# Kernel tuning notes

Hardware: AMD Instinct MI355X
Metric: run time of the kernel (lower is better)

Reference implementation:

```python
import jax, jax.numpy as jnp
import numpy as np

BN_EPS = 1e-5


def setup_inputs() -> dict:
    key = jax.random.key(0)
    ks = jax.random.split(key, 11)
    C, P = 256, 128  # inplanes, planes = inplanes // 2
    B, H, W = 4, 64, 64
    s = 0.01  # conv weight init std in the original module
    return {
        "x": jax.random.normal(ks[0], (B, C, H, W), jnp.float32),
        "Wt": jax.random.normal(ks[1], (P, C), jnp.float32) * s,
        "bt": jnp.zeros((P,), jnp.float32),
        "Wp": jax.random.normal(ks[2], (P, C), jnp.float32) * s,
        "bp": jnp.zeros((P,), jnp.float32),
        "Wg": jax.random.normal(ks[3], (P, C), jnp.float32) * s,
        "bg": jnp.zeros((P,), jnp.float32),
        "Wz": jax.random.normal(ks[4], (C, P), jnp.float32) * s,
        "bz": jnp.zeros((C,), jnp.float32),
        "gamma": jax.random.uniform(ks[5], (C,), jnp.float32),
        "beta": jax.random.normal(ks[6], (C,), jnp.float32) * 0.01,
    }


def reference(x, Wt, bt, Wp, bp, Wg, bg, Wz, bz, gamma, beta):
    b, c, h, w = x.shape
    n = h * w
    xf = x.reshape(b, c, n)  # (b, c, n)
    # 1x1 conv projections == per-pixel matmuls
    t = jnp.einsum("pc,bcn->bnp", Wt, xf) + bt            # (b, n, p) queries
    p = jnp.einsum("pc,bcn->bpn", Wp, xf) + bp[:, None]   # (b, p, n) keys
    g = jnp.einsum("pc,bcn->bnp", Wg, xf) + bg            # (b, n, p) values
    planes = Wt.shape[0]
    scale = jnp.asarray(planes, x.dtype) ** 0.5
    att = jnp.einsum("bnp,bpm->bnm", t, p) / scale        # (b, n, n)
    att = jax.nn.softmax(att, axis=-1)                    # softmax over dim 2
    y = jnp.einsum("bnm,bmp->bnp", att, g)                # (b, n, p)
    z = jnp.einsum("cp,bnp->bcn", Wz, y) + bz[:, None]    # (b, c, n)
    z = z.reshape(b, c, h, w)
    # BatchNorm2d, training-mode batch statistics over (B, H, W)
    mean = z.mean(axis=(0, 2, 3))
    var = z.var(axis=(0, 2, 3))
    zn = (z - mean[:, None, None]) * jax.lax.rsqrt(var + BN_EPS)[:, None, None]
    out = zn * gamma[:, None, None] + beta[:, None, None] + x
    return out
```

## Files before the change

kernel.cpp:

```cpp
#include <hip/hip_runtime.h>


#define SCALE_ 0.08838834764831845f
#define SCALE2_ 0.12752740475999508f

typedef __bf16 bf16x8 __attribute__((ext_vector_type(8)));
typedef float f32x4 __attribute__((ext_vector_type(4)));
typedef unsigned short ushort8v __attribute__((ext_vector_type(8)));

__device__ inline unsigned short f2bf(float f) {
  unsigned int u = __float_as_uint(f);
  u += 0x7fffu + ((u >> 16) & 1u);
  return (unsigned short)(u >> 16);
}
__device__ inline float bflo(unsigned int u) { return __uint_as_float(u << 16); }
__device__ inline float bfhi(unsigned int u) { return __uint_as_float(u & 0xffff0000u); }

__device__ inline void gl16(const unsigned short* g, unsigned short* l) {
  __builtin_amdgcn_global_load_lds(
      (const __attribute__((address_space(1))) unsigned int*)(g),
      (__attribute__((address_space(3))) unsigned int*)(l), 16, 0, 0);
}

__global__ __launch_bounds__(256) void prep_kernel(
    const float* __restrict__ x,
    const float* __restrict__ Wt, const float* __restrict__ Wp, const float* __restrict__ Wg,
    unsigned short* __restrict__ xT, unsigned short* __restrict__ Wb) {
  const int tid = threadIdx.x;
  const int bx = blockIdx.x, b = blockIdx.y;
  if (bx >= 64) {
    if (b != 0) return;
#pragma unroll
    for (int it = 0; it < 3; ++it) {
      int k = (bx - 64) * 256 + tid + it * 4096;
      const float* src = (k < 4096 ? Wt : (k < 8192 ? Wp : Wg)) + (size_t)(k & 4095) * 8;
      float4 a = *(const float4*)src, c = *(const float4*)(src + 4);
      ushort8v us;
      us[0] = f2bf(a.x); us[1] = f2bf(a.y); us[2] = f2bf(a.z); us[3] = f2bf(a.w);
      us[4] = f2bf(c.x); us[5] = f2bf(c.y); us[6] = f2bf(c.z); us[7] = f2bf(c.w);
      *(ushort8v*)(Wb + (size_t)k * 8) = us;
    }
    return;
  }
  __shared__ float sT[128 * 68];
  const int w = tid >> 6, l = tid & 63;
  const int n0 = bx * 64;
  for (int half = 0; half < 2; ++half) {
    if (half) __syncthreads();
#pragma unroll
    for (int it = 0; it < 8; ++it) {
      int e = it * 256 + tid;
      int c = e >> 4, n4 = e & 15;
      float4 v = *(const float4*)(x + (size_t)(b * 256 + half * 128 + c) * 4096 + n0 + n4 * 4);
      *(float4*)(sT + c * 68 + n4 * 4) = v;
    }
    __syncthreads();
#pragma unroll
    for (int it = 0; it < 4; ++it) {
      int c8 = it * 4 + w;
      int n = l;
      ushort8v us;
#pragma unroll
      for (int j = 0; j < 8; ++j) us[j] = f2bf(sT[(c8 * 8 + j) * 68 + n]);
      *(ushort8v*)(xT + (size_t)b * 1048576 + (size_t)(n0 + n) * 256 + half * 128 + c8 * 8) = us;
    }
  }
}

__global__ __launch_bounds__(256, 3) void proj_kernel(
    const unsigned short* __restrict__ xT, const unsigned short* __restrict__ Wb,
    const float* __restrict__ bt, const float* __restrict__ bp, const float* __restrict__ bg,
    unsigned short* __restrict__ Qb, unsigned short* __restrict__ Kb,
    unsigned short* __restrict__ Vtb) {
  __shared__ unsigned short sX[64 * 256];
  __shared__ unsigned short sW[128 * 64];
  const int tid = threadIdx.x;
  const int w = tid >> 6, l = tid & 63;
  const int l15 = l & 15, lh = l >> 4;
  const int n0 = blockIdx.x * 64;
  const int b = blockIdx.y;
  const int sel = blockIdx.z;
  const unsigned short* xTb = xT + (size_t)b * 1048576;
  const unsigned short* Ws = Wb + (size_t)sel * 32768;
#pragma unroll
  for (int it = 0; it < 8; ++it) {
    int row = w * 16 + it * 2 + (l >> 5);
    int s = l & 31;
    int src = (s & 24) | ((s & 7) ^ (row & 7));
    gl16(xTb + (size_t)(n0 + row) * 256 + src * 8, sX + (w * 16 + it * 2) * 256);
  }
  f32x4 acc[2][4];
#pragma unroll
  for (int mt = 0; mt < 2; ++mt)
#pragma unroll
    for (int nt = 0; nt < 4; ++nt) acc[mt][nt] = (f32x4){0.f, 0.f, 0.f, 0.f};

  for (int ko4 = 0; ko4 < 4; ++ko4) {
    __syncthreads();
#pragma unroll
    for (int it = 0; it < 4; ++it) {
      int p = w * 32 + it * 8 + (l >> 3);
      int s = l & 7;
      gl16(Ws + (size_t)p * 256 + ko4 * 64 + ((s ^ (p & 7)) * 8),
           sW + (w * 32 + it * 8) * 64);
    }
    __syncthreads();
#pragma unroll
    for (int ko2 = 0; ko2 < 2; ++ko2) {
      bf16x8 af[2];
#pragma unroll
      for (int mt = 0; mt < 2; ++mt) {
        int p = w * 32 + mt * 16 + l15;
        af[mt] = *(const bf16x8*)(sW + p * 64 + (((ko2 * 4 + lh) ^ (p & 7)) << 3));
      }
#pragma unroll
      for (int nt = 0; nt < 4; ++nt) {
        int n = nt * 16 + l15;
        int ci = ko4 * 8 + ko2 * 4 + lh;
        int slot = (ci & 24) | ((ci & 7) ^ (n & 7));
        bf16x8 bfv = *(const bf16x8*)(sX + n * 256 + (slot << 3));
#pragma unroll
        for (int mt = 0; mt < 2; ++mt)
          acc[mt][nt] = __builtin_amdgcn_mfma_f32_16x16x32_bf16(af[mt], bfv, acc[mt][nt], 0, 0, 0);
      }
    }
  }
  const float* bias = sel == 0 ? bt : (sel == 1 ? bp : bg);
  const float scl = sel == 0 ? SCALE2_ : 1.0f;
#pragma unroll
  for (int mt = 0; mt < 2; ++mt) {
    int pb = w * 32 + mt * 16 + lh * 4;
    float4 bv = *(const float4*)(bias + pb);
    const float* bvf = (const float*)&bv;
    if (sel < 2) {
      unsigned short* dst = (sel == 0 ? Qb : Kb) + (size_t)b * 524288;
#pragma unroll
      for (int nt = 0; nt < 4; ++nt) {
        ushort4 us;
        us.x = f2bf((acc[mt][nt][0] + bv.x) * scl);
        us.y = f2bf((acc[mt][nt][1] + bv.y) * scl);
        us.z = f2bf((acc[mt][nt][2] + bv.z) * scl);
        us.w = f2bf((acc[mt][nt][3] + bv.w) * scl);
        *(ushort4*)(dst + (size_t)(n0 + nt * 16 + l15) * 128 + pb) = us;
      }
    } else {
      unsigned short* dst = Vtb + (size_t)b * 524288;
#pragma unroll
      for (int nt = 0; nt < 4; ++nt)
#pragma unroll
        for (int r = 0; r < 4; ++r)
          dst[(size_t)(pb + r) * 4096 + n0 + nt * 16 + l15] = f2bf(acc[mt][nt][r] + bvf[r]);
    }
  }
}

__global__ __launch_bounds__(256, 2) void attn_kernel(
    const unsigned short* __restrict__ Qb, const unsigned short* __restrict__ Kb,
    const unsigned short* __restrict__ Vtb, unsigned short* __restrict__ Ytp,
    float* __restrict__ denp) {
  __shared__ unsigned short sm[40960];
  const int tid = threadIdx.x;
  const int w = tid >> 6, l = tid & 63;
  const int l15 = l & 15, lh = l >> 4;
  const int b = blockIdx.y, sp = blockIdx.z;
  const int n0 = blockIdx.x * 128;
  const int kvbase = sp * 1024;

  bf16x8 qf0[4], qf1[4];
  {
    const unsigned short* q0 = Qb + (size_t)(b * 4096 + n0 + w * 32 + l15) * 128 + lh * 8;
    const unsigned short* q1 = q0 + 16 * 128;
#pragma unroll
    for (int ko = 0; ko < 4; ++ko) {
      qf0[ko] = *(const bf16x8*)(q0 + ko * 32);
      qf1[ko] = *(const bf16x8*)(q1 + ko * 32);
    }
  }
  unsigned short* sPw = sm + 32768 + w * 2048;

  f32x4 yacc0[8], yacc1[8];
#pragma unroll
  for (int i = 0; i < 8; ++i) {
    yacc0[i] = (f32x4){0.f, 0.f, 0.f, 0.f};
    yacc1[i] = (f32x4){0.f, 0.f, 0.f, 0.f};
  }
  float den0 = 0.f, den1 = 0.f;

  const unsigned short* Kbase = Kb + (size_t)(b * 4096 + kvbase) * 128;
  const unsigned short* Vbase = Vtb + (size_t)(b * 128) * 4096 + kvbase;

#define STAGE(T, BUFO)                                                              \
  {                                                                                 \
    const int koff_ = (T) * 64;                                                     \
    _Pragma("unroll")                                                               \
    for (int it = 0; it < 4; ++it) {                                                \
      int krow = w * 16 + it * 4 + (l >> 4);                                        \
      gl16(Kbase + (size_t)(koff_ + krow) * 128 + (((l & 15) ^ (krow & 7)) << 3),   \
           sm + (BUFO) + (w * 16 + it * 4) * 128);                                  \
      int vrow = w * 32 + it * 8 + (l >> 3);                                        \
      gl16(Vbase + (size_t)vrow * 4096 + koff_ + (((l & 7) ^ (vrow & 7)) << 3),     \
           sm + 16384 + (BUFO) + (w * 32 + it * 8) * 64);                           \
    }                                                                               \
  }

  STAGE(0, 0)
  for (int t = 0; t < 16; ++t) {
    const int co = (t & 1) * 8192;
    unsigned short* kb = sm + co;
    unsigned short* vb = sm + 16384 + co;
    __syncthreads();
    if (t + 1 < 16) {
      STAGE(t + 1, co ^ 8192)
    }
    f32x4 sacc0[4], sacc1[4];
#pragma unroll
    for (int mt = 0; mt < 4; ++mt) {
      sacc0[mt] = (f32x4){0.f, 0.f, 0.f, 0.f};
      sacc1[mt] = (f32x4){0.f, 0.f, 0.f, 0.f};
    }
    __builtin_amdgcn_s_setprio(1);
#pragma unroll
    for (int ko = 0; ko < 4; ++ko) {
#pragma unroll
      for (int mt = 0; mt < 4; ++mt) {
        int m = mt * 16 + l15;
        bf16x8 ak = *(const bf16x8*)(kb + m * 128 + (((lh + 4 * ko) ^ (m & 7)) << 3));
        sacc0[mt] = __builtin_amdgcn_mfma_f32_16x16x32_bf16(ak, qf0[ko], sacc0[mt], 0, 0, 0);
        sacc1[mt] = __builtin_amdgcn_mfma_f32_16x16x32_bf16(ak, qf1[ko], sacc1[mt], 0, 0, 0);
      }
    }
    __builtin_amdgcn_s_setprio(0);
#define SOFTMAX_SET(SACC, ROWB, DEN)                                                \
    {                                                                               \
      float rs = 0.f;                                                               \
      _Pragma("unroll")                                                             \
      for (int mt = 0; mt < 4; ++mt) {                                              \
        float e0 = __builtin_amdgcn_exp2f(SACC[mt][0]);                             \
        float e1 = __builtin_amdgcn_exp2f(SACC[mt][1]);                             \
        float e2 = __builtin_amdgcn_exp2f(SACC[mt][2]);                             \
        float e3 = __builtin_amdgcn_exp2f(SACC[mt][3]);                             \
        rs += (e0 + e1) + (e2 + e3);                                                \
        unsigned ua, ub;                                                            \
        asm("v_cvt_pk_bf16_f32 %0, %1, %2" : "=v"(ua) : "v"(e0), "v"(e1));          \
        asm("v_cvt_pk_bf16_f32 %0, %1, %2" : "=v"(ub) : "v"(e2), "v"(e3));          \
        int mblk = mt * 2 + (lh >> 1);                                              \
        uint2 uv; uv.x = ua; uv.y = ub;                                             \
        *(uint2*)(sPw + ((ROWB) + l15) * 64 + ((mblk ^ (l15 & 7)) << 3) +           \
                  (lh & 1) * 4) = uv;                                               \
      }                                                                             \
      rs += __shfl_xor(rs, 16);                                                     \
      rs += __shfl_xor(rs, 32);                                                     \
      DEN += rs;                                                                    \
    }
    SOFTMAX_SET(sacc0, 0, den0)
    SOFTMAX_SET(sacc1, 16, den1)
    __builtin_amdgcn_s_setprio(1);
#pragma unroll
    for (int ko = 0; ko < 2; ++ko) {
      bf16x8 bp0 = *(const bf16x8*)(sPw + l15 * 64 + (((lh + 4 * ko) ^ (l15 & 7)) << 3));
      bf16x8 bp1 = *(const bf16x8*)(sPw + (16 + l15) * 64 + (((lh + 4 * ko) ^ (l15 & 7)) << 3));
#pragma unroll
      for (int dt = 0; dt < 8; ++dt) {
        int d = dt * 16 + l15;
        bf16x8 av = *(const bf16x8*)(vb + d * 64 + (((lh + 4 * ko) ^ (d & 7)) << 3));
        yacc0[dt] = __builtin_amdgcn_mfma_f32_16x16x32_bf16(av, bp0, yacc0[dt], 0, 0, 0);
        yacc1[dt] = __builtin_amdgcn_mfma_f32_16x16x32_bf16(av, bp1, yacc1[dt], 0, 0, 0);
      }
    }
    __builtin_amdgcn_s_setprio(0);
  }
  {
    unsigned short* Yt = Ytp + (size_t)(sp * 4 + b) * 524288 +
                         (size_t)(n0 + w * 32 + l15) * 128;
#pragma unroll
    for (int dt = 0; dt < 8; ++dt) {
      ushort4 us;
      us.x = f2bf(yacc0[dt][0]); us.y = f2bf(yacc0[dt][1]);
      us.z = f2bf(yacc0[dt][2]); us.w = f2bf(yacc0[dt][3]);
      *(ushort4*)(Yt + dt * 16 + lh * 4) = us;
    }
    unsigned short* Yt1 = Yt + 16 * 128;
#pragma unroll
    for (int dt = 0; dt < 8; ++dt) {
      ushort4 us;
      us.x = f2bf(yacc1[dt][0]); us.y = f2bf(yacc1[dt][1]);
      us.z = f2bf(yacc1[dt][2]); us.w = f2bf(yacc1[dt][3]);
      *(ushort4*)(Yt1 + dt * 16 + lh * 4) = us;
    }
    if (lh == 0) {
      denp[(size_t)(sp * 4 + b) * 4096 + n0 + w * 32 + l15] = den0;
      denp[(size_t)(sp * 4 + b) * 4096 + n0 + w * 32 + 16 + l15] = den1;
    }
  }
}

__global__ __launch_bounds__(256, 4) void zbn_kernel(
    const unsigned short* __restrict__ Ytp, const float* __restrict__ denp,
    const float* __restrict__ Wz, const float* __restrict__ bz,
    unsigned short* __restrict__ Zb, float* __restrict__ S1p, float* __restrict__ S2p) {
  __shared__ unsigned short sY[64 * 128];
  __shared__ unsigned short sW[64 * 128];
  __shared__ float sDen[64];
  const int tid = threadIdx.x;
  const int w = tid >> 6, l = tid & 63;
  const int l15 = l & 15, lh = l >> 4;
  const int bx = blockIdx.x;
  const int b = blockIdx.y;
  const int n0 = bx * 64;
  const int c0 = blockIdx.z * 64;
  if (tid < 64) {
    float s = 0.f;
#pragma unroll
    for (int sp = 0; sp < 4; ++sp) s += denp[sp * 16384 + b * 4096 + n0 + tid];
    sDen[tid] = 1.0f / s;
  }
  __syncthreads();
#pragma unroll
  for (int it = 0; it < 4; ++it) {
    int e = it * 256 + tid;
    int n = e >> 4, pc = e & 15;
    size_t o = (size_t)b * 524288 + (size_t)(n0 + n) * 128 + pc * 8;
    float a0 = 0, a1 = 0, a2 = 0, a3 = 0, a4 = 0, a5 = 0, a6 = 0, a7 = 0;
#pragma unroll
    for (int sp = 0; sp < 4; ++sp) {
      uint4 v = *(const uint4*)(Ytp + (size_t)sp * 2097152 + o);
      a0 += bflo(v.x); a1 += bfhi(v.x);
      a2 += bflo(v.y); a3 += bfhi(v.y);
      a4 += bflo(v.z); a5 += bfhi(v.z);
      a6 += bflo(v.w); a7 += bfhi(v.w);
    }
    float idn = sDen[n];
    ushort8v us;
    us[0] = f2bf(a0 * idn); us[1] = f2bf(a1 * idn);
    us[2] = f2bf(a2 * idn); us[3] = f2bf(a3 * idn);
    us[4] = f2bf(a4 * idn); us[5] = f2bf(a5 * idn);
    us[6] = f2bf(a6 * idn); us[7] = f2bf(a7 * idn);
    *(ushort8v*)(sY + n * 128 + ((pc ^ (n & 7)) << 3)) = us;
  }
#pragma unroll
  for (int it = 0; it < 4; ++it) {
    int e = it * 256 + tid;
    int c = e >> 4, pc = e & 15;
    const float* wsrc = Wz + (size_t)(c0 + c) * 128 + pc * 8;
    float4 wa = *(const float4*)(wsrc);
    float4 wb = *(const float4*)(wsrc + 4);
    ushort8v us;
    us[0] = f2bf(wa.x); us[1] = f2bf(wa.y); us[2] = f2bf(wa.z); us[3] = f2bf(wa.w);
    us[4] = f2bf(wb.x); us[5] = f2bf(wb.y); us[6] = f2bf(wb.z); us[7] = f2bf(wb.w);
    *(ushort8v*)(sW + c * 128 + ((pc ^ (c & 7)) << 3)) = us;
  }
  __syncthreads();
  f32x4 acc[4];
#pragma unroll
  for (int nt = 0; nt < 4; ++nt) acc[nt] = (f32x4){0.f, 0.f, 0.f, 0.f};
  const int crow = w * 16 + l15;
#pragma unroll
  for (int ko = 0; ko < 4; ++ko) {
    bf16x8 aw = *(const bf16x8*)(sW + crow * 128 + (((lh + 4 * ko) ^ (crow & 7)) << 3));
#pragma unroll
    for (int nt = 0; nt < 4; ++nt) {
      int nrow = nt * 16 + l15;
      bf16x8 by = *(const bf16x8*)(sY + nrow * 128 + (((lh + 4 * ko) ^ (nrow & 7)) << 3));
      acc[nt] = __builtin_amdgcn_mfma_f32_16x16x32_bf16(aw, by, acc[nt], 0, 0, 0);
    }
  }
  const int cb = c0 + w * 16 + lh * 4;
  float4 bzv = *(const float4*)(bz + cb);
  const float* bzf = (const float*)&bzv;
#pragma unroll
  for (int r = 0; r < 4; ++r) {
    float s1 = 0.f, s2 = 0.f;
#pragma unroll
    for (int nt = 0; nt < 4; ++nt) {
      float z = acc[nt][r] + bzf[r];
      Zb[(size_t)(b * 256 + cb + r) * 4096 + n0 + nt * 16 + l15] = f2bf(z);
      s1 += z;
      s2 += z * z;
    }
#pragma unroll
    for (int m = 1; m < 16; m <<= 1) {
      s1 += __shfl_xor(s1, m);
      s2 += __shfl_xor(s2, m);
    }
    if (l15 == 0) {
      S1p[(size_t)(cb + r) * 256 + b * 64 + bx] = s1;
      S2p[(size_t)(cb + r) * 256 + b * 64 + bx] = s2;
    }
  }
}

__global__ __launch_bounds__(256) void bnfin_kernel(
    const float* __restrict__ S1p, const float* __restrict__ S2p,
    const float* __restrict__ gamma, const float* __restrict__ beta,
    float* __restrict__ Scale, float* __restrict__ Shift) {
  __shared__ float r1[4], r2[4];
  const int c = blockIdx.x, tid = threadIdx.x;
  float s1 = S1p[(size_t)c * 256 + tid];
  float s2 = S2p[(size_t)c * 256 + tid];
#pragma unroll
  for (int m = 1; m < 64; m <<= 1) {
    s1 += __shfl_xor(s1, m);
    s2 += __shfl_xor(s2, m);
  }
  if ((tid & 63) == 0) { r1[tid >> 6] = s1; r2[tid >> 6] = s2; }
  __syncthreads();
  if (tid == 0) {
    float S1t = (r1[0] + r1[1]) + (r1[2] + r1[3]);
    float S2t = (r2[0] + r2[1]) + (r2[2] + r2[3]);
    const float inv_cnt = 1.0f / 16384.0f;
    float mean = S1t * inv_cnt;
    float var = fmaxf(S2t * inv_cnt - mean * mean, 0.0f);
    float inv = rsqrtf(var + 1e-5f);
    float sc = gamma[c] * inv;
    Scale[c] = sc;
    Shift[c] = beta[c] - mean * sc;
  }
}

__global__ __launch_bounds__(256) void out_kernel(
    const unsigned short* __restrict__ Zb, const float* __restrict__ x,
    const float* __restrict__ Scale, const float* __restrict__ Shift,
    float* __restrict__ out) {
  int i8 = blockIdx.x * 256 + threadIdx.x;
  size_t flat = (size_t)i8 * 8;
  int c = ((int)(flat >> 12)) & 255;
  uint4 zv = *(const uint4*)(Zb + flat);
  float4 xa = *(const float4*)(x + flat);
  float4 xb = *(const float4*)(x + flat + 4);
  float sc = Scale[c], sh = Shift[c];
  float4 oa, ob;
  oa.x = bflo(zv.x) * sc + sh + xa.x;
  oa.y = bfhi(zv.x) * sc + sh + xa.y;
  oa.z = bflo(zv.y) * sc + sh + xa.z;
  oa.w = bfhi(zv.y) * sc + sh + xa.w;
  ob.x = bflo(zv.z) * sc + sh + xb.x;
  ob.y = bfhi(zv.z) * sc + sh + xb.y;
  ob.z = bflo(zv.w) * sc + sh + xb.z;
  ob.w = bfhi(zv.w) * sc + sh + xb.w;
  *(float4*)(out + flat) = oa;
  *(float4*)(out + flat + 4) = ob;
}

extern "C" void kernel_launch(void* const* d_in, const int* in_sizes, int n_in,
                              void* d_out, int out_size, void* d_ws, size_t ws_size,
                              hipStream_t stream) {
  (void)in_sizes; (void)n_in; (void)out_size; (void)ws_size;
  const float* x = (const float*)d_in[0];
  const float* Wt = (const float*)d_in[1];
  const float* bt = (const float*)d_in[2];
  const float* Wp = (const float*)d_in[3];
  const float* bp = (const float*)d_in[4];
  const float* Wg = (const float*)d_in[5];
  const float* bg = (const float*)d_in[6];
  const float* Wz = (const float*)d_in[7];
  const float* bz = (const float*)d_in[8];
  const float* gamma = (const float*)d_in[9];
  const float* beta = (const float*)d_in[10];

  unsigned short* Qb = (unsigned short*)d_ws;
  unsigned short* Kb = Qb + 2097152;
  unsigned short* Vtb = Kb + 2097152;
  unsigned short* Ytp = Vtb + 2097152;
  float* denp = (float*)(Ytp + 8388608);
  float* Zr = denp + 65536;
  float* Scale = Zr + 4194304;
  float* Shift = Scale + 256;

  unsigned short* Zb = (unsigned short*)Zr;
  unsigned short* xT = (unsigned short*)Zr;
  unsigned short* Wb = (unsigned short*)denp;
  float* S1p = (float*)Qb;
  float* S2p = S1p + 65536;

  prep_kernel<<<dim3(80, 4), 256, 0, stream>>>(x, Wt, Wp, Wg, xT, Wb);
  proj_kernel<<<dim3(64, 4, 3), 256, 0, stream>>>(xT, Wb, bt, bp, bg, Qb, Kb, Vtb);
  attn_kernel<<<dim3(32, 4, 4), 256, 0, stream>>>(Qb, Kb, Vtb, Ytp, denp);
  zbn_kernel<<<dim3(64, 4, 4), 256, 0, stream>>>(Ytp, denp, Wz, bz, Zb, S1p, S2p);
  bnfin_kernel<<<256, 256, 0, stream>>>(S1p, S2p, gamma, beta, Scale, Shift);
  out_kernel<<<2048, 256, 0, stream>>>(Zb, x, Scale, Shift, (float*)d_out);
}
```

Baseline: 84.37 us.

## Switch attention Q/K/V and probabilities from bf16 to fp8 MFMA

Projection outputs Q, K and V^T are now quantized to FP8 (e4m3) instead of bf16, and the attention kernel uses fp8 16x16x32 MFMAs for both QK^T and PV, also packing softmax probabilities as fp8. Q is pre-scaled by a larger factor to use fp8 range, with a compensating 1/16 applied before exp2. This halves LDS and global traffic for K/V tiles, doubles matrix throughput, and raises the occupancy hint to 3 blocks. The cost is significant precision loss in the attention scores and weights, which may affect accuracy tolerance.

```diff
diff --git a/kernel.cpp b/kernel.cpp
--- a/kernel.cpp
+++ b/kernel.cpp
@@ -2,7 +2,7 @@
 
 
 #define SCALE_ 0.08838834764831845f
-#define SCALE2_ 0.12752740475999508f
+#define QSCALE_ 2.0404384761599213f
 
 typedef __bf16 bf16x8 __attribute__((ext_vector_type(8)));
 typedef float f32x4 __attribute__((ext_vector_type(4)));
@@ -16,7 +16,25 @@
 __device__ inline float bflo(unsigned int u) { return __uint_as_float(u << 16); }
 __device__ inline float bfhi(unsigned int u) { return __uint_as_float(u & 0xffff0000u); }
 
-__device__ inline void gl16(const unsigned short* g, unsigned short* l) {
+__device__ inline unsigned char f2fp8(float f) {
+  unsigned u = __float_as_uint(f);
+  unsigned sign = (u >> 24) & 0x80u;
+  unsigned a = u & 0x7fffffffu;
+  if (a >= 0x43E00000u) return (unsigned char)(sign | 0x7Eu);
+  if (a >= 0x3C800000u) {
+    unsigned r = a + 0x0007FFFFu + ((a >> 20) & 1u);
+    r &= 0xFFF00000u;
+    int e8 = (int)((r >> 23) & 0xFFu) - 120;
+    unsigned m3 = (r >> 20) & 7u;
+    return (unsigned char)(sign | ((unsigned)e8 << 3) | m3);
+  }
+  float q = __uint_as_float(a) * 512.0f;
+  int d = (int)rintf(q);
+  if (d >= 8) return (unsigned char)(sign | 0x08u);
+  return (unsigned char)(sign | (unsigned)d);
+}
+
+__device__ inline void gl16(const void* g, void* l) {
   __builtin_amdgcn_global_load_lds(
       (const __attribute__((address_space(1))) unsigned int*)(g),
       (__attribute__((address_space(3))) unsigned int*)(l), 16, 0, 0);
@@ -70,8 +88,8 @@
 __global__ __launch_bounds__(256, 3) void proj_kernel(
     const unsigned short* __restrict__ xT, const unsigned short* __restrict__ Wb,
     const float* __restrict__ bt, const float* __restrict__ bp, const float* __restrict__ bg,
-    unsigned short* __restrict__ Qb, unsigned short* __restrict__ Kb,
-    unsigned short* __restrict__ Vtb) {
+    unsigned char* __restrict__ Qb8, unsigned char* __restrict__ Kb8,
+    unsigned char* __restrict__ Vtb8) {
   __shared__ unsigned short sX[64 * 256];
   __shared__ unsigned short sW[128 * 64];
   const int tid = threadIdx.x;
@@ -126,39 +144,40 @@
     }
   }
   const float* bias = sel == 0 ? bt : (sel == 1 ? bp : bg);
-  const float scl = sel == 0 ? SCALE2_ : 1.0f;
+  const float scl = sel == 0 ? QSCALE_ : 1.0f;
 #pragma unroll
   for (int mt = 0; mt < 2; ++mt) {
     int pb = w * 32 + mt * 16 + lh * 4;
     float4 bv = *(const float4*)(bias + pb);
     const float* bvf = (const float*)&bv;
     if (sel < 2) {
-      unsigned short* dst = (sel == 0 ? Qb : Kb) + (size_t)b * 524288;
+      unsigned char* dst = (sel == 0 ? Qb8 : Kb8) + (size_t)b * 524288;
 #pragma unroll
       for (int nt = 0; nt < 4; ++nt) {
-        ushort4 us;
-        us.x = f2bf((acc[mt][nt][0] + bv.x) * scl);
-        us.y = f2bf((acc[mt][nt][1] + bv.y) * scl);
-        us.z = f2bf((acc[mt][nt][2] + bv.z) * scl);
-        us.w = f2bf((acc[mt][nt][3] + bv.w) * scl);
-        *(ushort4*)(dst + (size_t)(n0 + nt * 16 + l15) * 128 + pb) = us;
+        uchar4 us;
+        us.x = f2fp8((acc[mt][nt][0] + bv.x) * scl);
+        us.y = f2fp8((acc[mt][nt][1] + bv.y) * scl);
+        us.z = f2fp8((acc[mt][nt][2] + bv.z) * scl);
+        us.w = f2fp8((acc[mt][nt][3] + bv.w) * scl);
+        *(uchar4*)(dst + (size_t)(n0 + nt * 16 + l15) * 128 + pb) = us;
       }
     } else {
-      unsigned short* dst = Vtb + (size_t)b * 524288;
+      unsigned char* dst = Vtb8 + (size_t)b * 524288;
 #pragma unroll
       for (int nt = 0; nt < 4; ++nt)
 #pragma unroll
         for (int r = 0; r < 4; ++r)
-          dst[(size_t)(pb + r) * 4096 + n0 + nt * 16 + l15] = f2bf(acc[mt][nt][r] + bvf[r]);
-    }
-  }
-}
-
-__global__ __launch_bounds__(256, 2) void attn_kernel(
-    const unsigned short* __restrict__ Qb, const unsigned short* __restrict__ Kb,
-    const unsigned short* __restrict__ Vtb, unsigned short* __restrict__ Ytp,
+          dst[(size_t)(pb + r) * 4096 + n0 + nt * 16 + l15] = f2fp8(acc[mt][nt][r] + bvf[r]);
+    }
+  }
+}
+
+__global__ __launch_bounds__(256, 3) void attn_kernel(
+    const unsigned char* __restrict__ Qb8, const unsigned char* __restrict__ Kb8,
+    const unsigned char* __restrict__ Vtb8, unsigned short* __restrict__ Ytp,
     float* __restrict__ denp) {
-  __shared__ unsigned short sm[40960];
+  __shared__ long long smq[5120];
+  unsigned char* sm = (unsigned char*)smq;
   const int tid = threadIdx.x;
   const int w = tid >> 6, l = tid & 63;
   const int l15 = l & 15, lh = l >> 4;
@@ -166,17 +185,17 @@
   const int n0 = blockIdx.x * 128;
   const int kvbase = sp * 1024;
 
-  bf16x8 qf0[4], qf1[4];
+  long long qf0[4], qf1[4];
   {
-    const unsigned short* q0 = Qb + (size_t)(b * 4096 + n0 + w * 32 + l15) * 128 + lh * 8;
-    const unsigned short* q1 = q0 + 16 * 128;
+    const unsigned char* q0 = Qb8 + (size_t)(b * 4096 + n0 + w * 32 + l15) * 128 + lh * 8;
+    const unsigned char* q1 = q0 + 16 * 128;
 #pragma unroll
     for (int ko = 0; ko < 4; ++ko) {
-      qf0[ko] = *(const bf16x8*)(q0 + ko * 32);
-      qf1[ko] = *(const bf16x8*)(q1 + ko * 32);
-    }
-  }
-  unsigned short* sPw = sm + 32768 + w * 2048;
+      qf0[ko] = *(const long long*)(q0 + ko * 32);
+      qf1[ko] = *(const long long*)(q1 + ko * 32);
+    }
+  }
+  unsigned char* sPw = sm + 32768 + w * 2048;
 
   f32x4 yacc0[8], yacc1[8];
 #pragma unroll
@@ -186,28 +205,28 @@
   }
   float den0 = 0.f, den1 = 0.f;
 
-  const unsigned short* Kbase = Kb + (size_t)(b * 4096 + kvbase) * 128;
-  const unsigned short* Vbase = Vtb + (size_t)(b * 128) * 4096 + kvbase;
-
-#define STAGE(T, BUFO)                                                              \
-  {                                                                                 \
-    const int koff_ = (T) * 64;                                                     \
-    _Pragma("unroll")                                                               \
-    for (int it = 0; it < 4; ++it) {                                                \
-      int krow = w * 16 + it * 4 + (l >> 4);                                        \
-      gl16(Kbase + (size_t)(koff_ + krow) * 128 + (((l & 15) ^ (krow & 7)) << 3),   \
-           sm + (BUFO) + (w * 16 + it * 4) * 128);                                  \
-      int vrow = w * 32 + it * 8 + (l >> 3);                                        \
-      gl16(Vbase + (size_t)vrow * 4096 + koff_ + (((l & 7) ^ (vrow & 7)) << 3),     \
-           sm + 16384 + (BUFO) + (w * 32 + it * 8) * 64);                           \
-    }                                                                               \
+  const unsigned char* Kbase = Kb8 + (size_t)(b * 4096 + kvbase) * 128;
+  const unsigned char* Vbase = Vtb8 + (size_t)(b * 128) * 4096 + kvbase;
+
+#define STAGE(T, BUFO)                                                               \
+  {                                                                                  \
+    const int koff_ = (T) * 64;                                                      \
+    _Pragma("unroll")                                                                \
+    for (int it = 0; it < 2; ++it) {                                                 \
+      int krow = w * 16 + it * 8 + (l >> 3);                                         \
+      gl16(Kbase + (size_t)(koff_ + krow) * 128 + (((l & 7) ^ (krow & 7)) << 4),     \
+           sm + (BUFO) + (w * 16 + it * 8) * 128);                                   \
+      int vrow = w * 32 + it * 16 + (l >> 2);                                        \
+      gl16(Vbase + (size_t)vrow * 4096 + koff_ + (((l & 3) ^ (vrow & 3)) << 4),      \
+           sm + 16384 + (BUFO) + (w * 32 + it * 16) * 64);                           \
+    }                                                                                \
   }
 
   STAGE(0, 0)
   for (int t = 0; t < 16; ++t) {
     const int co = (t & 1) * 8192;
-    unsigned short* kb = sm + co;
-    unsigned short* vb = sm + 16384 + co;
+    unsigned char* kb = sm + co;
+    unsigned char* vb = sm + 16384 + co;
     __syncthreads();
     if (t + 1 < 16) {
       STAGE(t + 1, co ^ 8192)
@@ -224,47 +243,48 @@
 #pragma unroll
       for (int mt = 0; mt < 4; ++mt) {
         int m = mt * 16 + l15;
-        bf16x8 ak = *(const bf16x8*)(kb + m * 128 + (((lh + 4 * ko) ^ (m & 7)) << 3));
-        sacc0[mt] = __builtin_amdgcn_mfma_f32_16x16x32_bf16(ak, qf0[ko], sacc0[mt], 0, 0, 0);
-        sacc1[mt] = __builtin_amdgcn_mfma_f32_16x16x32_bf16(ak, qf1[ko], sacc1[mt], 0, 0, 0);
+        long long ak = *(const long long*)(
+            kb + m * 128 + (((ko * 4 + lh) ^ ((m & 7) << 1)) << 3));
+        sacc0[mt] = __builtin_amdgcn_mfma_f32_16x16x32_fp8_fp8(ak, qf0[ko], sacc0[mt], 0, 0, 0);
+        sacc1[mt] = __builtin_amdgcn_mfma_f32_16x16x32_fp8_fp8(ak, qf1[ko], sacc1[mt], 0, 0, 0);
       }
     }
     __builtin_amdgcn_s_setprio(0);
-#define SOFTMAX_SET(SACC, ROWB, DEN)                                                \
-    {                                                                               \
-      float rs = 0.f;                                                               \
-      _Pragma("unroll")                                                             \
-      for (int mt = 0; mt < 4; ++mt) {                                              \
-        float e0 = __builtin_amdgcn_exp2f(SACC[mt][0]);                             \
-        float e1 = __builtin_amdgcn_exp2f(SACC[mt][1]);                             \
-        float e2 = __builtin_amdgcn_exp2f(SACC[mt][2]);                             \
-        float e3 = __builtin_amdgcn_exp2f(SACC[mt][3]);                             \
-        rs += (e0 + e1) + (e2 + e3);                                                \
-        unsigned ua, ub;                                                            \
-        asm("v_cvt_pk_bf16_f32 %0, %1, %2" : "=v"(ua) : "v"(e0), "v"(e1));          \
-        asm("v_cvt_pk_bf16_f32 %0, %1, %2" : "=v"(ub) : "v"(e2), "v"(e3));          \
-        int mblk = mt * 2 + (lh >> 1);                                              \
-        uint2 uv; uv.x = ua; uv.y = ub;                                             \
-        *(uint2*)(sPw + ((ROWB) + l15) * 64 + ((mblk ^ (l15 & 7)) << 3) +           \
-                  (lh & 1) * 4) = uv;                                               \
-      }                                                                             \
-      rs += __shfl_xor(rs, 16);                                                     \
-      rs += __shfl_xor(rs, 32);                                                     \
-      DEN += rs;                                                                    \
+#define SOFTMAX_SET(SACC, ROWB, DEN)                                                 \
+    {                                                                                \
+      float rs = 0.f;                                                                \
+      _Pragma("unroll")                                                              \
+      for (int mt = 0; mt < 4; ++mt) {                                               \
+        float e0 = __builtin_amdgcn_exp2f(SACC[mt][0] * 0.0625f);                    \
+        float e1 = __builtin_amdgcn_exp2f(SACC[mt][1] * 0.0625f);                    \
+        float e2 = __builtin_amdgcn_exp2f(SACC[mt][2] * 0.0625f);                    \
+        float e3 = __builtin_amdgcn_exp2f(SACC[mt][3] * 0.0625f);                    \
+        rs += (e0 + e1) + (e2 + e3);                                                 \
+        int pk = __builtin_amdgcn_cvt_pk_fp8_f32(e0, e1, 0, false);                  \
+        pk = __builtin_amdgcn_cvt_pk_fp8_f32(e2, e3, pk, true);                      \
+        *(int*)(sPw + ((ROWB) + l15) * 64 +                                          \
+                (((mt * 2 + (lh >> 1)) ^ (l15 & 7)) << 3) + (lh & 1) * 4) = pk;      \
+      }                                                                              \
+      rs += __shfl_xor(rs, 16);                                                      \
+      rs += __shfl_xor(rs, 32);                                                      \
+      DEN += rs;                                                                     \
     }
     SOFTMAX_SET(sacc0, 0, den0)
     SOFTMAX_SET(sacc1, 16, den1)
     __builtin_amdgcn_s_setprio(1);
 #pragma unroll
     for (int ko = 0; ko < 2; ++ko) {
-      bf16x8 bp0 = *(const bf16x8*)(sPw + l15 * 64 + (((lh + 4 * ko) ^ (l15 & 7)) << 3));
-      bf16x8 bp1 = *(const bf16x8*)(sPw + (16 + l15) * 64 + (((lh + 4 * ko) ^ (l15 & 7)) << 3));
+      long long bp0 = *(const long long*)(
+          sPw + l15 * 64 + (((ko * 4 + lh) ^ (l15 & 7)) << 3));
+      long long bp1 = *(const long long*)(
+          sPw + (16 + l15) * 64 + (((ko * 4 + lh) ^ (l15 & 7)) << 3));
 #pragma unroll
       for (int dt = 0; dt < 8; ++dt) {
         int d = dt * 16 + l15;
-        bf16x8 av = *(const bf16x8*)(vb + d * 64 + (((lh + 4 * ko) ^ (d & 7)) << 3));
-        yacc0[dt] = __builtin_amdgcn_mfma_f32_16x16x32_bf16(av, bp0, yacc0[dt], 0, 0, 0);
-        yacc1[dt] = __builtin_amdgcn_mfma_f32_16x16x32_bf16(av, bp1, yacc1[dt], 0, 0, 0);
+        long long av = *(const long long*)(
+            vb + d * 64 + (((ko * 4 + lh) ^ ((d & 3) << 1)) << 3));
+        yacc0[dt] = __builtin_amdgcn_mfma_f32_16x16x32_fp8_fp8(av, bp0, yacc0[dt], 0, 0, 0);
+        yacc1[dt] = __builtin_amdgcn_mfma_f32_16x16x32_fp8_fp8(av, bp1, yacc1[dt], 0, 0, 0);
       }
     }
     __builtin_amdgcn_s_setprio(0);
@@ -457,10 +477,10 @@
   const float* gamma = (const float*)d_in[9];
   const float* beta = (const float*)d_in[10];
 
-  unsigned short* Qb = (unsigned short*)d_ws;
-  unsigned short* Kb = Qb + 2097152;
-  unsigned short* Vtb = Kb + 2097152;
-  unsigned short* Ytp = Vtb + 2097152;
+  unsigned char* Qb8 = (unsigned char*)d_ws;
+  unsigned char* Kb8 = Qb8 + 2097152;
+  unsigned char* Vtb8 = Kb8 + 2097152;
+  unsigned short* Ytp = (unsigned short*)(Vtb8 + 2097152);
   float* denp = (float*)(Ytp + 8388608);
   float* Zr = denp + 65536;
   float* Scale = Zr + 4194304;
@@ -469,12 +489,12 @@
   unsigned short* Zb = (unsigned short*)Zr;
   unsigned short* xT = (unsigned short*)Zr;
   unsigned short* Wb = (unsigned short*)denp;
-  float* S1p = (float*)Qb;
+  float* S1p = (float*)Qb8;
   float* S2p = S1p + 65536;
 
   prep_kernel<<<dim3(80, 4), 256, 0, stream>>>(x, Wt, Wp, Wg, xT, Wb);
-  proj_kernel<<<dim3(64, 4, 3), 256, 0, stream>>>(xT, Wb, bt, bp, bg, Qb, Kb, Vtb);
-  attn_kernel<<<dim3(32, 4, 4), 256, 0, stream>>>(Qb, Kb, Vtb, Ytp, denp);
+  proj_kernel<<<dim3(64, 4, 3), 256, 0, stream>>>(xT, Wb, bt, bp, bg, Qb8, Kb8, Vtb8);
+  attn_kernel<<<dim3(32, 4, 4), 256, 0, stream>>>(Qb8, Kb8, Vtb8, Ytp, denp);
   zbn_kernel<<<dim3(64, 4, 4), 256, 0, stream>>>(Ytp, denp, Wz, bz, Zb, S1p, S2p);
   bnfin_kernel<<<256, 256, 0, stream>>>(S1p, S2p, gamma, beta, Scale, Shift);
   out_kernel<<<2048, 256, 0, stream>>>(Zb, x, Scale, Shift, (float*)d_out);
```

Measured after the change: 86.12 us. 2.1% more time.
